# Kernel tuning notes

Hardware: AMD Instinct MI355X
Metric: run time of the kernel (lower is better)

Reference implementation:

```python
import jax, jax.numpy as jnp
import numpy as np


def setup_inputs() -> dict:
    B, Lq, Lk, D, F, H = 2, 2048, 2048, 128, 128, 8
    key = jax.random.key(0)
    ks = jax.random.split(key, 8)
    X_Q = jax.random.normal(ks[0], (B, Lq, D), dtype=jnp.float32)
    X_K = jax.random.normal(ks[1], (B, Lk, D), dtype=jnp.float32)
    X_V = jax.random.normal(ks[2], (B, Lk, F), dtype=jnp.float32)
    mask = jax.random.randint(ks[3], (B, 1, Lq, Lk), 0, 2, dtype=jnp.int32)
    # xavier_normal for [H, D, D]: std = sqrt(2/(D+D))
    W_Q = jax.random.normal(ks[4], (H, D, D), dtype=jnp.float32) * np.sqrt(2.0 / (D + D))
    W_K = jax.random.normal(ks[5], (H, D, D), dtype=jnp.float32) * np.sqrt(2.0 / (D + D))
    W_V = jax.random.normal(ks[6], (H, F, F), dtype=jnp.float32) * np.sqrt(2.0 / (F + F))
    O = jax.random.normal(ks[7], (F * H, F), dtype=jnp.float32) * np.sqrt(2.0 / (F * H + F))
    return {"X_Q": X_Q, "X_K": X_K, "X_V": X_V, "mask": mask,
            "W_Q": W_Q, "W_K": W_K, "W_V": W_V, "O": O}


def reference(X_Q, X_K, X_V, mask, W_Q, W_K, W_V, O):
    B, Lq, D = X_Q.shape
    H = W_Q.shape[0]
    F = W_V.shape[1]
    # torch.einsum with repeated in-operand index ('hdd') takes the diagonal
    dq = jnp.diagonal(W_Q, axis1=1, axis2=2)  # [H, D]
    dk = jnp.diagonal(W_K, axis1=1, axis2=2)  # [H, D]
    dv = jnp.diagonal(W_V, axis1=1, axis2=2)  # [H, F]
    g = dq * dk                               # fused per-head QK diagonal scale [H, D]
    scale = 1.0 / jnp.sqrt(jnp.asarray(D, dtype=X_Q.dtype))
    scores = jnp.einsum('bqd,hd,bkd->bhqk', X_Q, g, X_K) * scale  # [B,H,Lq,Lk]
    scores = jnp.where(mask == 0, jnp.asarray(-jnp.inf, scores.dtype), scores)
    A = jax.nn.softmax(scores, axis=-1)
    # O_h = A @ (diag(dv_h) scaled V)
    Oh = jnp.einsum('bhqk,hf,bkf->bhqf', A, dv, X_V)  # [B,H,Lq,F]
    Oh = Oh.transpose(0, 2, 1, 3).reshape(B, Lq, H * F)
    return jnp.einsum('bqx,xf->bqf', Oh, O)
```

## Files before the change

kernel.cpp:

```cpp
#include <hip/hip_runtime.h>

typedef __bf16 bf16;
typedef __bf16 bf16x4 __attribute__((ext_vector_type(4)));
typedef __bf16 bf16x8 __attribute__((ext_vector_type(8)));
typedef float f32x4 __attribute__((ext_vector_type(4)));
typedef unsigned int u32;
typedef unsigned long long u64;

#define B_ 2
#define H_ 8
#define L_ 2048
#define D_ 128
#define F_ 128
#define QT 64
#define KT 64
#define NKT (L_ / KT)

#define WS_KB 0u
#define WS_VT (1u << 20)
#define WS_MB (2u << 20)

#define SMEM_BYTES 75776
#define SP_OFF 65536
#define SP_STRIDE 72
#define LWS_OFF 74752
#define SOH_STRIDE 136
#define SO2_STRIDE 136

__device__ __forceinline__ void dma16(const void* g, void* l) {
    __builtin_amdgcn_global_load_lds(
        (const __attribute__((address_space(1))) u32*)g,
        (__attribute__((address_space(3))) u32*)l, 16, 0, 0);
}

__global__ __launch_bounds__(256)
void prep_all(const float* __restrict__ XK, const float* __restrict__ XV,
              const int* __restrict__ mask, bf16* __restrict__ Kb,
              bf16* __restrict__ Vtb, u64* __restrict__ bits)
{
    const int bid = blockIdx.x;
    const int tid = threadIdx.x;
    if (bid < 8192) {
        int wv = bid * 4 + (tid >> 6);
        int lane = tid & 63;
        size_t base = (size_t)wv * 256;
        #pragma unroll
        for (int s = 0; s < 4; ++s) {
            int m = mask[base + s * 64 + lane];
            u64 bal = __ballot(m != 0);
            if (lane == 0) bits[(size_t)wv * 4 + s] = bal;
        }
    } else if (bid < 8448) {
        int gid = (bid - 8192) * 256 + tid;
        int row = gid >> 4;
        int j   = gid & 15;
        const float* src = XK + (size_t)row * 128 + j * 8;
        float4 v0 = *(const float4*)src;
        float4 v1 = *(const float4*)(src + 4);
        bf16x8 w;
        w[0] = (bf16)v0.x; w[1] = (bf16)v0.y; w[2] = (bf16)v0.z; w[3] = (bf16)v0.w;
        w[4] = (bf16)v1.x; w[5] = (bf16)v1.y; w[6] = (bf16)v1.z; w[7] = (bf16)v1.w;
        int jp = j ^ (row & 15);
        *(bf16x8*)(Kb + (size_t)row * 128 + jp * 8) = w;
    } else {
        int idx  = bid - 8448;
        int tile = idx >> 2;
        int fq   = idx & 3;
        int f    = fq * 32 + (tid & 31);
        int j    = tid >> 5;
        int bb   = tile >> 5, kt = tile & 31;
        const float* src = XV + ((size_t)(bb * L_ + kt * 64 + j * 8)) * F_ + f;
        bf16x8 w;
        #pragma unroll
        for (int jj = 0; jj < 8; ++jj) w[jj] = (bf16)src[(size_t)jj * F_];
        *(bf16x8*)(Vtb + (size_t)tile * 8192 + f * 64 + ((j ^ (f & 7)) * 8)) = w;
    }
}

__global__ __launch_bounds__(512, 4)
void attn_fused_kernel(const float* __restrict__ XQ, const bf16* __restrict__ Kb,
                       const bf16* __restrict__ Vtb, const u64* __restrict__ bits,
                       const float* __restrict__ WQ, const float* __restrict__ WK,
                       const float* __restrict__ WV, const float* __restrict__ Om,
                       float* __restrict__ out)
{
    __shared__ __align__(16) char smem[SMEM_BYTES];
    __shared__ __align__(16) float g_s[128];

    bf16* sK0 = (bf16*)smem;
    bf16* sK1 = (bf16*)(smem + 16384);
    bf16* sV0 = (bf16*)(smem + 32768);
    bf16* sV1 = (bf16*)(smem + 49152);
    bf16* sP  = (bf16*)(smem + SP_OFF);
    float* lws = (float*)(smem + LWS_OFF);
    bf16* sOh  = (bf16*)smem;
    bf16* sO2t = (bf16*)(smem + 17408);

    const int tid  = threadIdx.x;
    const int wave = tid >> 6;
    const int lane = tid & 63;
    const int c    = lane & 15;
    const int quad = lane >> 4;
    const int qt = blockIdx.x, h = blockIdx.y, b = blockIdx.z;
    const int q0 = qt * QT;

    const int kq   = wave & 3;
    const int msel = wave >> 2;
    const int mq = wave & 3;
    const int fh = wave >> 2;
    const int fv  = tid & 127;
    const int grp = tid >> 7;

    if (tid < 128) {
        float wq = WQ[(h * D_ + tid) * D_ + tid];
        float wk = WK[(h * D_ + tid) * D_ + tid];
        g_s[tid] = wq * wk * 0.08838834764831845f;
    }
    __syncthreads();

    const char* gKbase = (const char*)Kb + (size_t)(b * L_) * 256;
    const char* gVbase = (const char*)Vtb + (size_t)(b * NKT) * 16384;

    #pragma unroll
    for (int i = 0; i < 2; ++i) dma16(gKbase + i * 8192 + tid * 16, (char*)sK0 + i * 8192 + tid * 16);
    #pragma unroll
    for (int i = 0; i < 2; ++i) dma16(gVbase + i * 8192 + tid * 16, (char*)sV0 + i * 8192 + tid * 16);

    bf16x8 qfrag[2][4];
    #pragma unroll
    for (int mi = 0; mi < 2; ++mi) {
        const float* qrow = XQ + (size_t)(b * L_ + q0 + (msel * 2 + mi) * 16 + c) * D_;
        #pragma unroll
        for (int kc = 0; kc < 4; ++kc) {
            int d0 = kc * 32 + quad * 8;
            float4 v0 = *(const float4*)(qrow + d0);
            float4 v1 = *(const float4*)(qrow + d0 + 4);
            float4 g0 = *(const float4*)(g_s + d0);
            float4 g1 = *(const float4*)(g_s + d0 + 4);
            bf16x8 w;
            w[0] = (bf16)(v0.x * g0.x); w[1] = (bf16)(v0.y * g0.y);
            w[2] = (bf16)(v0.z * g0.z); w[3] = (bf16)(v0.w * g0.w);
            w[4] = (bf16)(v1.x * g1.x); w[5] = (bf16)(v1.y * g1.y);
            w[6] = (bf16)(v1.z * g1.z); w[7] = (bf16)(v1.w * g1.w);
            qfrag[mi][kc] = w;
        }
    }

    f32x4 oacc[4];
    #pragma unroll
    for (int fi = 0; fi < 4; ++fi)
        #pragma unroll
        for (int r = 0; r < 4; ++r) oacc[fi][r] = 0.f;
    float lsum[2] = {0.f, 0.f};

    const int shift = kq * 16 + quad * 4;

    #pragma unroll 2
    for (int kt = 0; kt < NKT; ++kt) {
        bf16* sK  = (kt & 1) ? sK1 : sK0;
        bf16* sV  = (kt & 1) ? sV1 : sV0;
        bf16* sKn = (kt & 1) ? sK0 : sK1;
        bf16* sVn = (kt & 1) ? sV0 : sV1;

        asm volatile("s_barrier" ::: "memory");

        u64 mb[2];
        #pragma unroll
        for (int mi = 0; mi < 2; ++mi)
            mb[mi] = bits[(size_t)(b * L_ + q0 + (msel * 2 + mi) * 16 + c) * NKT + kt];

        if (kt + 1 < NKT) {
            const char* gk = gKbase + (size_t)(kt + 1) * 16384;
            const char* gv = gVbase + (size_t)(kt + 1) * 16384;
            #pragma unroll
            for (int i = 0; i < 2; ++i) dma16(gk + i * 8192 + tid * 16, (char*)sKn + i * 8192 + tid * 16);
            #pragma unroll
            for (int i = 0; i < 2; ++i) dma16(gv + i * 8192 + tid * 16, (char*)sVn + i * 8192 + tid * 16);
            asm volatile("s_waitcnt vmcnt(6)" ::: "memory");
        } else {
            asm volatile("s_waitcnt vmcnt(2)" ::: "memory");
        }
        asm volatile("s_barrier" ::: "memory");

        f32x4 tacc[2];
        #pragma unroll
        for (int mi = 0; mi < 2; ++mi)
            #pragma unroll
            for (int r = 0; r < 4; ++r) tacc[mi][r] = 0.f;

        const bf16* krow = sK + (kq * 16 + c) * 128;
        #pragma unroll
        for (int kc = 0; kc < 4; ++kc) {
            bf16x8 kfrag = *(const bf16x8*)(krow + (((kc * 4 + quad) ^ c) * 8));
            #pragma unroll
            for (int mi = 0; mi < 2; ++mi)
                tacc[mi] = __builtin_amdgcn_mfma_f32_16x16x32_bf16(kfrag, qfrag[mi][kc], tacc[mi], 0, 0, 0);
        }

        #pragma unroll
        for (int mi = 0; mi < 2; ++mi) {
            bf16x4 pw;
            #pragma unroll
            for (int r = 0; r < 4; ++r) {
                float p = ((mb[mi] >> (shift + r)) & 1ull) ? __expf(tacc[mi][r]) : 0.f;
                lsum[mi] += p;
                pw[r] = (bf16)p;
            }
            *(bf16x4*)(sP + ((msel * 2 + mi) * 16 + c) * SP_STRIDE + shift) = pw;
        }
        asm volatile("s_waitcnt lgkmcnt(0)" ::: "memory");
        asm volatile("s_barrier" ::: "memory");

        #pragma unroll
        for (int kc = 0; kc < 2; ++kc) {
            bf16x8 pfrag = *(const bf16x8*)(sP + (mq * 16 + c) * SP_STRIDE + kc * 32 + quad * 8);
            #pragma unroll
            for (int fi = 0; fi < 4; ++fi) {
                const bf16* vrow = sV + ((fh * 4 + fi) * 16 + c) * 64;
                bf16x8 vfrag = *(const bf16x8*)(vrow + (((kc * 4 + quad) ^ (c & 7)) * 8));
                oacc[fi] = __builtin_amdgcn_mfma_f32_16x16x32_bf16(pfrag, vfrag, oacc[fi], 0, 0, 0);
            }
        }
    }

    #pragma unroll
    for (int mi = 0; mi < 2; ++mi) {
        float v = lsum[mi];
        v += __shfl_xor(v, 16); v += __shfl_xor(v, 32);
        if (lane < 16) lws[wave * 32 + mi * 16 + lane] = v;
    }
    __syncthreads();

    if (tid < 128)
        g_s[tid] = WV[(h * F_ + tid) * F_ + tid];

    float linv[4];
    #pragma unroll
    for (int r = 0; r < 4; ++r) {
        int cc = quad * 4 + r;
        int base = (mq >> 1) * 4;
        int off  = (mq & 1) * 16 + cc;
        float s = lws[(base + 0) * 32 + off] + lws[(base + 1) * 32 + off]
                + lws[(base + 2) * 32 + off] + lws[(base + 3) * 32 + off];
        linv[r] = 1.0f / s;
    }
    #pragma unroll
    for (int fi = 0; fi < 4; ++fi)
        #pragma unroll
        for (int r = 0; r < 4; ++r) {
            int q_local = mq * 16 + quad * 4 + r;
            int f_col   = (fh * 4 + fi) * 16 + c;
            sOh[q_local * SOH_STRIDE + f_col] = (bf16)(oacc[fi][r] * linv[r]);
        }
    __syncthreads();

    #pragma unroll
    for (int i = 0; i < 8; ++i) {
        int fp4 = grp * 32 + i * 4;
        bf16x4 w;
        #pragma unroll
        for (int j = 0; j < 4; ++j) {
            int x = fp4 + j;
            w[j] = (bf16)(Om[(h * F_ + x) * F_ + fv] * g_s[x]);
        }
        *(bf16x4*)(sO2t + fv * SO2_STRIDE + fp4) = w;
    }
    __syncthreads();

    const int pm = wave & 3;
    const int pf = wave >> 2;
    bf16x8 afr[4];
    const bf16* ohrow = sOh + (pm * 16 + c) * SOH_STRIDE;
    #pragma unroll
    for (int kc = 0; kc < 4; ++kc)
        afr[kc] = *(const bf16x8*)(ohrow + kc * 32 + quad * 8);

    #pragma unroll
    for (int nt = 0; nt < 4; ++nt) {
        f32x4 pacc;
        #pragma unroll
        for (int r = 0; r < 4; ++r) pacc[r] = 0.f;
        const bf16* orow = sO2t + ((pf * 4 + nt) * 16 + c) * SO2_STRIDE;
        #pragma unroll
        for (int kc = 0; kc < 4; ++kc) {
            bf16x8 bfrag = *(const bf16x8*)(orow + kc * 32 + quad * 8);
            pacc = __builtin_amdgcn_mfma_f32_16x16x32_bf16(afr[kc], bfrag, pacc, 0, 0, 0);
        }
        #pragma unroll
        for (int r = 0; r < 4; ++r) {
            int qg = q0 + pm * 16 + quad * 4 + r;
            atomicAdd(out + ((size_t)(b * L_ + qg) * F_ + (pf * 4 + nt) * 16 + c), pacc[r]);
        }
    }
}

extern "C" void kernel_launch(void* const* d_in, const int* in_sizes, int n_in,
                              void* d_out, int out_size, void* d_ws, size_t ws_size,
                              hipStream_t stream) {
    const float* XQ   = (const float*)d_in[0];
    const float* XK   = (const float*)d_in[1];
    const float* XV   = (const float*)d_in[2];
    const int*   mask = (const int*)d_in[3];
    const float* WQ   = (const float*)d_in[4];
    const float* WK   = (const float*)d_in[5];
    const float* WV   = (const float*)d_in[6];
    const float* Om   = (const float*)d_in[7];
    float* out = (float*)d_out;

    char* ws = (char*)d_ws;
    bf16* Kb   = (bf16*)(ws + WS_KB);
    bf16* Vtb  = (bf16*)(ws + WS_VT);
    u64*  bits = (u64*)(ws + WS_MB);

    prep_all<<<8704, 256, 0, stream>>>(XK, XV, mask, Kb, Vtb, bits);
    hipMemsetAsync(out, 0, (size_t)out_size * sizeof(float), stream);

    dim3 grid(L_ / QT, H_, B_);
    attn_fused_kernel<<<grid, 512, 0, stream>>>(XQ, Kb, Vtb, bits, WQ, WK, WV, Om, out);
}
```

Baseline: 165.5 us.

## Keep P in registers via 16x16x16 MFMA, split keys across wave halves

Reassigns waves so each wave owns one 16-row query slice and half of each key tile. The exp'd scores stay in registers as the A operand of 16x16x16 bf16 MFMAs against V, which removes the shared-memory P buffer and one barrier per key tile. V is repacked in 4-element swizzled groups to match the new fragment layout. Partial outputs from the two key halves are reduced through shared memory at the end. In exchange, oacc doubles to 8 accumulators per wave, which raises register pressure, and the smaller-K MFMA issues more instructions.

```diff
diff --git a/kernel.cpp b/kernel.cpp
--- a/kernel.cpp
+++ b/kernel.cpp
@@ -4,6 +4,7 @@
 typedef __bf16 bf16x4 __attribute__((ext_vector_type(4)));
 typedef __bf16 bf16x8 __attribute__((ext_vector_type(8)));
 typedef float f32x4 __attribute__((ext_vector_type(4)));
+typedef short s16x4 __attribute__((ext_vector_type(4)));
 typedef unsigned int u32;
 typedef unsigned long long u64;
 
@@ -20,10 +21,10 @@
 #define WS_VT (1u << 20)
 #define WS_MB (2u << 20)
 
-#define SMEM_BYTES 75776
-#define SP_OFF 65536
-#define SP_STRIDE 72
-#define LWS_OFF 74752
+#define SMEM_BYTES 66048
+#define LWS_OFF 65536
+#define POX_STRIDE 132
+#define SOH_OFF 36864
 #define SOH_STRIDE 136
 #define SO2_STRIDE 136
 
@@ -31,6 +32,20 @@
     __builtin_amdgcn_global_load_lds(
         (const __attribute__((address_space(1))) u32*)g,
         (__attribute__((address_space(3))) u32*)l, 16, 0, 0);
+}
+
+__device__ __forceinline__ f32x4 mfma32(bf16x8 a, bf16x8 b, f32x4 c) {
+    return __builtin_amdgcn_mfma_f32_16x16x32_bf16(a, b, c, 0, 0, 0);
+}
+
+__device__ __forceinline__ f32x4 mfma16(bf16x4 a, bf16x4 b, f32x4 c) {
+#if __has_builtin(__builtin_amdgcn_mfma_f32_16x16x16_bf16)
+    return __builtin_amdgcn_mfma_f32_16x16x16_bf16(a, b, c, 0, 0, 0);
+#else
+    s16x4 as = __builtin_bit_cast(s16x4, a);
+    s16x4 bs = __builtin_bit_cast(s16x4, b);
+    return __builtin_amdgcn_mfma_f32_16x16x16bf16_1k(as, bs, c, 0, 0, 0);
+#endif
 }
 
 __global__ __launch_bounds__(256)
@@ -70,10 +85,15 @@
         int j    = tid >> 5;
         int bb   = tile >> 5, kt = tile & 31;
         const float* src = XV + ((size_t)(bb * L_ + kt * 64 + j * 8)) * F_ + f;
-        bf16x8 w;
-        #pragma unroll
-        for (int jj = 0; jj < 8; ++jj) w[jj] = (bf16)src[(size_t)jj * F_];
-        *(bf16x8*)(Vtb + (size_t)tile * 8192 + f * 64 + ((j ^ (f & 7)) * 8)) = w;
+        bf16x4 w0, w1;
+        #pragma unroll
+        for (int jj = 0; jj < 4; ++jj) {
+            w0[jj] = (bf16)src[(size_t)jj * F_];
+            w1[jj] = (bf16)src[(size_t)(4 + jj) * F_];
+        }
+        bf16* outp = Vtb + (size_t)tile * 8192 + f * 64;
+        *(bf16x4*)(outp + (((2 * j) ^ (f & 15)) * 4)) = w0;
+        *(bf16x4*)(outp + (((2 * j + 1) ^ (f & 15)) * 4)) = w1;
     }
 }
 
@@ -91,10 +111,10 @@
     bf16* sK1 = (bf16*)(smem + 16384);
     bf16* sV0 = (bf16*)(smem + 32768);
     bf16* sV1 = (bf16*)(smem + 49152);
-    bf16* sP  = (bf16*)(smem + SP_OFF);
     float* lws = (float*)(smem + LWS_OFF);
-    bf16* sOh  = (bf16*)smem;
-    bf16* sO2t = (bf16*)(smem + 17408);
+    float* pOx = (float*)smem;
+    bf16* sOh  = (bf16*)(smem + SOH_OFF);
+    bf16* sO2t = (bf16*)smem;
 
     const int tid  = threadIdx.x;
     const int wave = tid >> 6;
@@ -104,10 +124,8 @@
     const int qt = blockIdx.x, h = blockIdx.y, b = blockIdx.z;
     const int q0 = qt * QT;
 
-    const int kq   = wave & 3;
-    const int msel = wave >> 2;
-    const int mq = wave & 3;
-    const int fh = wave >> 2;
+    const int kh   = wave >> 2;
+    const int msel = wave & 3;
     const int fv  = tid & 127;
     const int grp = tid >> 7;
 
@@ -126,10 +144,9 @@
     #pragma unroll
     for (int i = 0; i < 2; ++i) dma16(gVbase + i * 8192 + tid * 16, (char*)sV0 + i * 8192 + tid * 16);
 
-    bf16x8 qfrag[2][4];
-    #pragma unroll
-    for (int mi = 0; mi < 2; ++mi) {
-        const float* qrow = XQ + (size_t)(b * L_ + q0 + (msel * 2 + mi) * 16 + c) * D_;
+    bf16x8 qfrag[4];
+    {
+        const float* qrow = XQ + (size_t)(b * L_ + q0 + msel * 16 + c) * D_;
         #pragma unroll
         for (int kc = 0; kc < 4; ++kc) {
             int d0 = kc * 32 + quad * 8;
@@ -142,18 +159,18 @@
             w[2] = (bf16)(v0.z * g0.z); w[3] = (bf16)(v0.w * g0.w);
             w[4] = (bf16)(v1.x * g1.x); w[5] = (bf16)(v1.y * g1.y);
             w[6] = (bf16)(v1.z * g1.z); w[7] = (bf16)(v1.w * g1.w);
-            qfrag[mi][kc] = w;
-        }
-    }
-
-    f32x4 oacc[4];
-    #pragma unroll
-    for (int fi = 0; fi < 4; ++fi)
+            qfrag[kc] = w;
+        }
+    }
+
+    f32x4 oacc[8];
+    #pragma unroll
+    for (int fi = 0; fi < 8; ++fi)
         #pragma unroll
         for (int r = 0; r < 4; ++r) oacc[fi][r] = 0.f;
-    float lsum[2] = {0.f, 0.f};
-
-    const int shift = kq * 16 + quad * 4;
+    float lsum = 0.f;
+
+    const u64* mrow = bits + (size_t)(b * L_ + q0 + msel * 16 + c) * NKT;
 
     #pragma unroll 2
     for (int kt = 0; kt < NKT; ++kt) {
@@ -164,10 +181,7 @@
 
         asm volatile("s_barrier" ::: "memory");
 
-        u64 mb[2];
-        #pragma unroll
-        for (int mi = 0; mi < 2; ++mi)
-            mb[mi] = bits[(size_t)(b * L_ + q0 + (msel * 2 + mi) * 16 + c) * NKT + kt];
+        u64 mb = mrow[kt];
 
         if (kt + 1 < NKT) {
             const char* gk = gKbase + (size_t)(kt + 1) * 16384;
@@ -176,82 +190,85 @@
             for (int i = 0; i < 2; ++i) dma16(gk + i * 8192 + tid * 16, (char*)sKn + i * 8192 + tid * 16);
             #pragma unroll
             for (int i = 0; i < 2; ++i) dma16(gv + i * 8192 + tid * 16, (char*)sVn + i * 8192 + tid * 16);
-            asm volatile("s_waitcnt vmcnt(6)" ::: "memory");
+            asm volatile("s_waitcnt vmcnt(5)" ::: "memory");
         } else {
-            asm volatile("s_waitcnt vmcnt(2)" ::: "memory");
+            asm volatile("s_waitcnt vmcnt(1)" ::: "memory");
         }
         asm volatile("s_barrier" ::: "memory");
 
         f32x4 tacc[2];
         #pragma unroll
-        for (int mi = 0; mi < 2; ++mi)
-            #pragma unroll
-            for (int r = 0; r < 4; ++r) tacc[mi][r] = 0.f;
-
-        const bf16* krow = sK + (kq * 16 + c) * 128;
-        #pragma unroll
-        for (int kc = 0; kc < 4; ++kc) {
-            bf16x8 kfrag = *(const bf16x8*)(krow + (((kc * 4 + quad) ^ c) * 8));
-            #pragma unroll
-            for (int mi = 0; mi < 2; ++mi)
-                tacc[mi] = __builtin_amdgcn_mfma_f32_16x16x32_bf16(kfrag, qfrag[mi][kc], tacc[mi], 0, 0, 0);
-        }
-
-        #pragma unroll
-        for (int mi = 0; mi < 2; ++mi) {
-            bf16x4 pw;
+        for (int kti = 0; kti < 2; ++kti)
+            #pragma unroll
+            for (int r = 0; r < 4; ++r) tacc[kti][r] = 0.f;
+
+        #pragma unroll
+        for (int kti = 0; kti < 2; ++kti) {
+            const bf16* krow = sK + ((kh * 2 + kti) * 16 + c) * 128;
+            #pragma unroll
+            for (int kc = 0; kc < 4; ++kc) {
+                bf16x8 kfrag = *(const bf16x8*)(krow + (((kc * 4 + quad) ^ c) * 8));
+                tacc[kti] = mfma32(kfrag, qfrag[kc], tacc[kti]);
+            }
+        }
+
+        bf16x4 pfrag[2];
+        #pragma unroll
+        for (int kti = 0; kti < 2; ++kti) {
             #pragma unroll
             for (int r = 0; r < 4; ++r) {
-                float p = ((mb[mi] >> (shift + r)) & 1ull) ? __expf(tacc[mi][r]) : 0.f;
-                lsum[mi] += p;
-                pw[r] = (bf16)p;
+                float p = ((mb >> (kh * 32 + kti * 16 + quad * 4 + r)) & 1ull)
+                          ? __expf(tacc[kti][r]) : 0.f;
+                lsum += p;
+                pfrag[kti][r] = (bf16)p;
             }
-            *(bf16x4*)(sP + ((msel * 2 + mi) * 16 + c) * SP_STRIDE + shift) = pw;
-        }
-        asm volatile("s_waitcnt lgkmcnt(0)" ::: "memory");
-        asm volatile("s_barrier" ::: "memory");
-
-        #pragma unroll
-        for (int kc = 0; kc < 2; ++kc) {
-            bf16x8 pfrag = *(const bf16x8*)(sP + (mq * 16 + c) * SP_STRIDE + kc * 32 + quad * 8);
-            #pragma unroll
-            for (int fi = 0; fi < 4; ++fi) {
-                const bf16* vrow = sV + ((fh * 4 + fi) * 16 + c) * 64;
-                bf16x8 vfrag = *(const bf16x8*)(vrow + (((kc * 4 + quad) ^ (c & 7)) * 8));
-                oacc[fi] = __builtin_amdgcn_mfma_f32_16x16x32_bf16(pfrag, vfrag, oacc[fi], 0, 0, 0);
+        }
+
+        #pragma unroll
+        for (int fi = 0; fi < 8; ++fi) {
+            #pragma unroll
+            for (int kti = 0; kti < 2; ++kti) {
+                int g = kh * 8 + kti * 4 + quad;
+                bf16x4 vfrag = *(const bf16x4*)(sV + (fi * 16 + c) * 64 + ((g ^ c) * 4));
+                oacc[fi] = mfma16(pfrag[kti], vfrag, oacc[fi]);
             }
         }
     }
 
-    #pragma unroll
-    for (int mi = 0; mi < 2; ++mi) {
-        float v = lsum[mi];
+    {
+        float v = lsum;
         v += __shfl_xor(v, 16); v += __shfl_xor(v, 32);
-        if (lane < 16) lws[wave * 32 + mi * 16 + lane] = v;
-    }
-    __syncthreads();
-
+        if (lane < 16) lws[wave * 16 + lane] = v;
+    }
     if (tid < 128)
         g_s[tid] = WV[(h * F_ + tid) * F_ + tid];
-
-    float linv[4];
-    #pragma unroll
-    for (int r = 0; r < 4; ++r) {
-        int cc = quad * 4 + r;
-        int base = (mq >> 1) * 4;
-        int off  = (mq & 1) * 16 + cc;
-        float s = lws[(base + 0) * 32 + off] + lws[(base + 1) * 32 + off]
-                + lws[(base + 2) * 32 + off] + lws[(base + 3) * 32 + off];
-        linv[r] = 1.0f / s;
-    }
-    #pragma unroll
-    for (int fi = 0; fi < 4; ++fi)
+    __syncthreads();
+
+    if (kh == 1) {
+        #pragma unroll
+        for (int fi = 0; fi < 8; ++fi)
+            #pragma unroll
+            for (int r = 0; r < 4; ++r)
+                pOx[(msel * 16 + quad * 4 + r) * POX_STRIDE + fi * 16 + c] = oacc[fi][r];
+    }
+    __syncthreads();
+
+    if (kh == 0) {
+        float linv[4];
         #pragma unroll
         for (int r = 0; r < 4; ++r) {
-            int q_local = mq * 16 + quad * 4 + r;
-            int f_col   = (fh * 4 + fi) * 16 + c;
-            sOh[q_local * SOH_STRIDE + f_col] = (bf16)(oacc[fi][r] * linv[r]);
-        }
+            int m16 = quad * 4 + r;
+            linv[r] = 1.0f / (lws[msel * 16 + m16] + lws[(4 + msel) * 16 + m16]);
+        }
+        #pragma unroll
+        for (int fi = 0; fi < 8; ++fi)
+            #pragma unroll
+            for (int r = 0; r < 4; ++r) {
+                int row = msel * 16 + quad * 4 + r;
+                float v = (oacc[fi][r] + pOx[row * POX_STRIDE + fi * 16 + c]) * linv[r];
+                sOh[row * SOH_STRIDE + fi * 16 + c] = (bf16)v;
+            }
+    }
     __syncthreads();
 
     #pragma unroll
@@ -284,7 +301,7 @@
         #pragma unroll
         for (int kc = 0; kc < 4; ++kc) {
             bf16x8 bfrag = *(const bf16x8*)(orow + kc * 32 + quad * 8);
-            pacc = __builtin_amdgcn_mfma_f32_16x16x32_bf16(afr[kc], bfrag, pacc, 0, 0, 0);
+            pacc = mfma32(afr[kc], bfrag, pacc);
         }
         #pragma unroll
         for (int r = 0; r < 4; ++r) {
```

Result: faster. 156.0 us (-5.7%).
